# Performance work log

Hardware: AMD Instinct MI355X
Metric: run time of the kernel (lower is better)

The kernel has to match this reference:

```python
import jax, jax.numpy as jnp
import numpy as np
from jax.scipy.special import logsumexp

DEN_SCALE = 1.0  # den_scale from LFMMILoss.__init__


def _log_marginal(em, seqlens, logA, log_start, log_final):
    """Forward (alpha) recursion of a WFSA in log space.
    em: [B,T,S] per-state emission log-likelihoods; logA: [S,S] or [B,S,S].
    Returns per-sequence log-marginal [B].
    """
    B, T, S = em.shape
    alpha0 = log_start + em[:, 0]  # [B,S]

    def step(alpha, xs):
        em_t, t = xs
        # [B,S,1] + [.,S,S] -> logsumexp over source state
        new = logsumexp(alpha[:, :, None] + logA, axis=1) + em_t
        alpha = jnp.where((t < seqlens)[:, None], new, alpha)
        return alpha, None

    em_t_first = jnp.swapaxes(em, 0, 1)  # [T,B,S]
    alpha, _ = jax.lax.scan(step, alpha0, (em_t_first[1:], jnp.arange(1, T)))
    return logsumexp(alpha + log_final, axis=1)  # [B]


def _fsm_logprob(x, seqlens, logA, log_start, log_final, pdf_ids):
    B, T, _ = x.shape
    if pdf_ids.ndim == 1:  # shared graph (denominator)
        em = x[:, :, pdf_ids]  # [B,T,S]
    else:  # per-utterance graphs (numerators), pdf_ids: [B,S]
        S = pdf_ids.shape[-1]
        idx = jnp.broadcast_to(pdf_ids[:, None, :], (B, T, S))
        em = jnp.take_along_axis(x, idx, axis=2)
    return _log_marginal(em, seqlens, logA, log_start, log_final)


def setup_inputs() -> dict:
    key = jax.random.key(0)
    ks = jax.random.split(key, 10)
    B, T, C = 16, 500, 2048
    S_num, S_den = 64, 512
    inp = jax.random.normal(ks[0], (B, T, C), jnp.float32)
    seqlengths = jax.random.randint(ks[1], (B,), T // 2, T + 1, jnp.int32)
    num_logA = jax.nn.log_softmax(jax.random.normal(ks[2], (B, S_num, S_num), jnp.float32), axis=-1)
    num_log_start = jax.nn.log_softmax(jax.random.normal(ks[3], (B, S_num), jnp.float32), axis=-1)
    num_log_final = jax.nn.log_softmax(jax.random.normal(ks[4], (B, S_num), jnp.float32), axis=-1)
    num_pdf_ids = jax.random.randint(ks[5], (B, S_num), 0, C, jnp.int32)
    den_logA = jax.nn.log_softmax(jax.random.normal(ks[6], (S_den, S_den), jnp.float32), axis=-1)
    den_log_start = jax.nn.log_softmax(jax.random.normal(ks[7], (S_den,), jnp.float32), axis=-1)
    den_log_final = jax.nn.log_softmax(jax.random.normal(ks[8], (S_den,), jnp.float32), axis=-1)
    den_pdf_ids = jax.random.randint(ks[9], (S_den,), 0, C, jnp.int32)
    return {
        "input": inp, "seqlengths": seqlengths,
        "num_logA": num_logA, "num_log_start": num_log_start,
        "num_log_final": num_log_final, "num_pdf_ids": num_pdf_ids,
        "den_logA": den_logA, "den_log_start": den_log_start,
        "den_log_final": den_log_final, "den_pdf_ids": den_pdf_ids,
    }


def reference(input, seqlengths, num_logA, num_log_start, num_log_final,
              num_pdf_ids, den_logA, den_log_start, den_log_final, den_pdf_ids):
    x = jnp.clip(input, -30.0, 30.0)
    num_llh = _fsm_logprob(x, seqlengths, num_logA, num_log_start, num_log_final, num_pdf_ids).sum()
    den_llh = _fsm_logprob(x, seqlengths, den_logA, den_log_start, den_log_final, den_pdf_ids).sum()
    return -(num_llh - DEN_SCALE * den_llh)
```

## Files before the change

kernel.cpp:

```cpp
#include <hip/hip_runtime.h>
#include <math.h>

#define BB 16
#define TT 500
#define CC 2048
#define SN 64
#define SD 512
#define NDEN 128
#define NTHR 512
#define SHIFTC 30.0f

#define WSF_DACC   32768
#define WSF_DSCALE 32784
#define WSF_NACC   32800
#define WSF_NSCALE 32816

#define AL(p) __hip_atomic_load((p), __ATOMIC_RELAXED, __HIP_MEMORY_SCOPE_AGENT)
#define AS(p, v) __hip_atomic_store((p), (v), __ATOMIC_RELAXED, __HIP_MEMORY_SCOPE_AGENT)

__device__ __forceinline__ float wave_max(float v) {
  #pragma unroll
  for (int off = 32; off > 0; off >>= 1) v = fmaxf(v, __shfl_xor(v, off, 64));
  return v;
}
__device__ __forceinline__ float wave_sum(float v) {
  #pragma unroll
  for (int off = 32; off > 0; off >>= 1) v += __shfl_xor(v, off, 64);
  return v;
}
__device__ __forceinline__ unsigned long long pk(unsigned tag, float v) {
  return ((unsigned long long)tag << 32) | (unsigned long long)__float_as_uint(v);
}
__device__ __forceinline__ float clamp30(float v) {
  return fminf(fmaxf(v, -30.f), 30.f);
}

__global__ __launch_bounds__(NTHR, 1) void fsm_fwd(
    const float* __restrict__ x, const int* __restrict__ seqlens,
    const float* __restrict__ nA, const float* __restrict__ nls,
    const float* __restrict__ nlf, const int* __restrict__ npdf,
    const float* __restrict__ dA, const float* __restrict__ dls,
    const float* __restrict__ dlf, const int* __restrict__ dpdf,
    unsigned long long* __restrict__ p64, float* __restrict__ wsf)
{
  __shared__ float prt[2][8][64];
  __shared__ float pmx[2][8];
  const int tid = threadIdx.x;
  const int lane = tid & 63, wv = tid >> 6;

  if (blockIdx.x < NDEN) {
    const int g  = blockIdx.x & 15;
    const int cb = blockIdx.x >> 4;
    const int j0 = cb * 64;

    float Areg[64];
    {
      const float* Ap = dA + (size_t)(wv * 64) * SD + j0 + lane;
      #pragma unroll
      for (int k = 0; k < 64; ++k)
        Areg[k] = __expf(Ap[(size_t)k * SD]);
    }

    unsigned long long* gb0 = p64 + (size_t)g * SD;
    unsigned long long* gb1 = p64 + (size_t)(16 + g) * SD;

    const int si = j0 + lane;
    int pdfj = 0, sl = 0; float lfj = 0.f, pcur = 0.f, scale = SHIFTC;
    const float* xb = x + (size_t)g * TT * CC;
    if (wv == 0) {
      pdfj = dpdf[si];
      lfj  = dlf[si];
      sl   = seqlens[g];
      float xv = clamp30(xb[pdfj]);
      pcur = __expf(dls[si] + xv - SHIFTC);
      AS(gb0 + si, pk(0u, pcur));
    }
    float lmlag = 0.f;

    for (int t = 1; t < TT; ++t) {
      unsigned long long* gin  = (t & 1) ? gb0 : gb1;
      unsigned long long* gout = (t & 1) ? gb1 : gb0;

      float emfac = 0.f;
      if (wv == 0) {
        float xq = clamp30(xb[(size_t)t * CC + pdfj]);
        emfac = __expf(xq - SHIFTC - lmlag);
      }

      const unsigned tg = (unsigned)(t - 1);
      unsigned long long* pa = gin + wv * 64 + lane;
      float pwin;
      {
        unsigned long long w = AL(pa);
        for (;;) {
          unsigned long long wn = AL(pa);
          if ((unsigned)(w >> 32) == tg) {
            pwin = __uint_as_float((unsigned)w);
            break;
          }
          __builtin_amdgcn_s_sleep(1);
          w = wn;
        }
      }

      float q = 0.f;
      #pragma unroll
      for (int k = 0; k < 64; ++k) {
        float pv = __uint_as_float(__builtin_amdgcn_readlane(__float_as_uint(pwin), k));
        q = fmaf(pv, Areg[k], q);
      }
      prt[t & 1][wv][lane] = q;
      float cm = wave_max(pwin);
      if (lane == 0) pmx[t & 1][wv] = cm;
      __syncthreads();

      if (wv == 0) {
        float s = 0.f;
        #pragma unroll
        for (int r = 0; r < 8; ++r) s += prt[t & 1][r][lane];
        if (t < sl) {
          pcur = s * emfac;
          scale += SHIFTC + lmlag;
        }
        AS(gout + si, pk((unsigned)t, pcur));
        float m = pmx[t & 1][0];
        #pragma unroll
        for (int r = 1; r < 8; ++r) m = fmaxf(m, pmx[t & 1][r]);
        lmlag = __logf(m);
      }
    }
    if (wv == 0) {
      float part = wave_sum(pcur * __expf(lfj));
      if (lane == 0) {
        atomicAdd(wsf + WSF_DACC + g, part);
        if (cb == 0) wsf[WSF_DSCALE + g] = scale;
      }
    }
  } else {
    const int b = blockIdx.x - NDEN;
    if (wv != 0) return;

    float Areg[64];
    {
      const float* Ap = nA + b * SN * SN + lane;
      #pragma unroll
      for (int i = 0; i < 64; ++i)
        Areg[i] = __expf(Ap[i * SN]);
    }
    const int   pdfj = npdf[b * SN + lane];
    const float lfj  = nlf[b * SN + lane];
    const int   sl   = seqlens[b];
    float xv = clamp30(x[(size_t)b * TT * CC + pdfj]);
    float pcur = __expf(nls[b * SN + lane] + xv - SHIFTC);
    float scale = SHIFTC;

    for (int t = 1; t < TT; ++t) {
      xv = clamp30(x[(size_t)b * TT * CC + t * CC + pdfj]);
      float pold = pcur;
      float q = 0.f;
      #pragma unroll
      for (int i = 0; i < 64; ++i) {
        float pi = __uint_as_float(__builtin_amdgcn_readlane(__float_as_uint(pold), i));
        q = fmaf(pi, Areg[i], q);
      }
      float lm = __logf(wave_max(pold));
      if (t < sl) {
        pcur = q * __expf(xv - SHIFTC - lm);
        scale += SHIFTC + lm;
      }
    }
    float part = wave_sum(pcur * __expf(lfj));
    if (lane == 0) {
      wsf[WSF_NACC + b]   = part;
      wsf[WSF_NSCALE + b] = scale;
    }
  }
}

__global__ void fsm_final(const float* __restrict__ wsf, float* __restrict__ out) {
  const int tid = threadIdx.x;
  float v = 0.f;
  if (tid < 16)
    v = -(wsf[WSF_NSCALE + tid] + __logf(wsf[WSF_NACC + tid]));
  else if (tid < 32)
    v = (wsf[WSF_DSCALE + tid - 16] + __logf(wsf[WSF_DACC + tid - 16]));
  v = wave_sum(v);
  if (tid == 0) out[0] = v;
}

extern "C" void kernel_launch(void* const* d_in, const int* in_sizes, int n_in,
                              void* d_out, int out_size, void* d_ws, size_t ws_size,
                              hipStream_t stream) {
  const float* x    = (const float*)d_in[0];
  const int*   sql  = (const int*)d_in[1];
  const float* nA   = (const float*)d_in[2];
  const float* nls  = (const float*)d_in[3];
  const float* nlf  = (const float*)d_in[4];
  const int*   npdf = (const int*)d_in[5];
  const float* dA   = (const float*)d_in[6];
  const float* dls  = (const float*)d_in[7];
  const float* dlf  = (const float*)d_in[8];
  const int*   dpdf = (const int*)d_in[9];
  float* out = (float*)d_out;
  unsigned long long* p64 = (unsigned long long*)d_ws;
  float* wsf = (float*)d_ws;
  (void)in_sizes; (void)n_in; (void)out_size; (void)ws_size;

  hipMemsetAsync((char*)d_ws + 131072, 0, 256, stream);
  fsm_fwd<<<NDEN + BB, NTHR, 0, stream>>>(x, sql, nA, nls, nlf, npdf,
                                          dA, dls, dlf, dpdf, p64, wsf);
  fsm_final<<<1, 64, 0, stream>>>(wsf, out);
}
```

Baseline: 932.9 us.

## Add fast SE-scope exchange path with device-scope fallback for cross-block alpha handoff

Each denominator timestep's alpha values are now written twice: to a buffer using sc0 (shader-engine/L2-near) stores and to a device-scope buffer using sc1. Consumers poll the fast buffer first and fall back to the device-scope copy every few spins. Fast buffers are initialised with a sentinel tag. The goal is lower latency in the per-step inter-block handoff, which sets the pace of the serial recursion. The cost is an extra store per step and reliance on cache-coherence semantics that depend on which blocks share a shader engine.

After: 1.132 ms. 21.3% more time.

```diff
diff --git a/kernel.cpp b/kernel.cpp
--- a/kernel.cpp
+++ b/kernel.cpp
@@ -9,14 +9,32 @@
 #define NDEN 128
 #define NTHR 512
 #define SHIFTC 30.0f
-
-#define WSF_DACC   32768
-#define WSF_DSCALE 32784
-#define WSF_NACC   32800
-#define WSF_NSCALE 32816
-
-#define AL(p) __hip_atomic_load((p), __ATOMIC_RELAXED, __HIP_MEMORY_SCOPE_AGENT)
-#define AS(p, v) __hip_atomic_store((p), (v), __ATOMIC_RELAXED, __HIP_MEMORY_SCOPE_AGENT)
+#define SENT 0xFFFFFFFF00000000ull
+
+#define SLOWO 16384
+#define WSF_DACC   65536
+#define WSF_DSCALE 65552
+#define WSF_NACC   65568
+#define WSF_NSCALE 65584
+
+__device__ __forceinline__ void st_se(unsigned long long* p, unsigned long long v) {
+  asm volatile("global_store_dwordx2 %0, %1, off sc0" :: "v"(p), "v"(v) : "memory");
+}
+__device__ __forceinline__ unsigned long long ld_se(const unsigned long long* p) {
+  unsigned long long r;
+  asm volatile("global_load_dwordx2 %0, %1, off sc0\n\ts_waitcnt vmcnt(0)"
+               : "=v"(r) : "v"(p) : "memory");
+  return r;
+}
+__device__ __forceinline__ void st_dev(unsigned long long* p, unsigned long long v) {
+  asm volatile("global_store_dwordx2 %0, %1, off sc1" :: "v"(p), "v"(v) : "memory");
+}
+__device__ __forceinline__ unsigned long long ld_dev(const unsigned long long* p) {
+  unsigned long long r;
+  asm volatile("global_load_dwordx2 %0, %1, off sc1\n\ts_waitcnt vmcnt(0)"
+               : "=v"(r) : "v"(p) : "memory");
+  return r;
+}
 
 __device__ __forceinline__ float wave_max(float v) {
   #pragma unroll
@@ -53,6 +71,14 @@
     const int cb = blockIdx.x >> 4;
     const int j0 = cb * 64;
 
+    unsigned long long* fb0 = p64 + (size_t)g * SD;
+    unsigned long long* fb1 = p64 + (size_t)(16 + g) * SD;
+    unsigned long long* sb0 = p64 + SLOWO + (size_t)g * SD;
+    unsigned long long* sb1 = p64 + SLOWO + (size_t)(16 + g) * SD;
+
+    st_se(fb0 + wv * 64 + lane, SENT);
+    st_se(fb1 + wv * 64 + lane, SENT);
+
     float Areg[64];
     {
       const float* Ap = dA + (size_t)(wv * 64) * SD + j0 + lane;
@@ -60,9 +86,7 @@
       for (int k = 0; k < 64; ++k)
         Areg[k] = __expf(Ap[(size_t)k * SD]);
     }
-
-    unsigned long long* gb0 = p64 + (size_t)g * SD;
-    unsigned long long* gb1 = p64 + (size_t)(16 + g) * SD;
+    __syncthreads();
 
     const int si = j0 + lane;
     int pdfj = 0, sl = 0; float lfj = 0.f, pcur = 0.f, scale = SHIFTC;
@@ -73,13 +97,16 @@
       sl   = seqlens[g];
       float xv = clamp30(xb[pdfj]);
       pcur = __expf(dls[si] + xv - SHIFTC);
-      AS(gb0 + si, pk(0u, pcur));
+      st_dev(sb0 + si, pk(0u, pcur));
     }
     float lmlag = 0.f;
 
     for (int t = 1; t < TT; ++t) {
-      unsigned long long* gin  = (t & 1) ? gb0 : gb1;
-      unsigned long long* gout = (t & 1) ? gb1 : gb0;
+      const int bi = t & 1;
+      unsigned long long* fin  = bi ? fb0 : fb1;
+      unsigned long long* sin  = bi ? sb0 : sb1;
+      unsigned long long* fout = bi ? fb1 : fb0;
+      unsigned long long* sout = bi ? sb1 : sb0;
 
       float emfac = 0.f;
       if (wv == 0) {
@@ -88,44 +115,54 @@
       }
 
       const unsigned tg = (unsigned)(t - 1);
-      unsigned long long* pa = gin + wv * 64 + lane;
-      float pwin;
-      {
-        unsigned long long w = AL(pa);
+      unsigned long long* fa = fin + wv * 64 + lane;
+      unsigned long long* sa = sin + wv * 64 + lane;
+      unsigned long long w;
+      if (t == 1) {
         for (;;) {
-          unsigned long long wn = AL(pa);
-          if ((unsigned)(w >> 32) == tg) {
-            pwin = __uint_as_float((unsigned)w);
-            break;
+          w = ld_dev(sa);
+          if ((unsigned)(w >> 32) == tg) break;
+          __builtin_amdgcn_s_sleep(1);
+        }
+      } else {
+        int k = 0;
+        for (;;) {
+          w = ld_se(fa);
+          if ((unsigned)(w >> 32) == tg) break;
+          if ((++k & 3) == 0) {
+            w = ld_dev(sa);
+            if ((unsigned)(w >> 32) == tg) break;
+            __builtin_amdgcn_s_sleep(1);
           }
-          __builtin_amdgcn_s_sleep(1);
-          w = wn;
         }
       }
+      float pwin = __uint_as_float((unsigned)w);
 
       float q = 0.f;
       #pragma unroll
-      for (int k = 0; k < 64; ++k) {
-        float pv = __uint_as_float(__builtin_amdgcn_readlane(__float_as_uint(pwin), k));
-        q = fmaf(pv, Areg[k], q);
-      }
-      prt[t & 1][wv][lane] = q;
+      for (int k2 = 0; k2 < 64; ++k2) {
+        float pv = __uint_as_float(__builtin_amdgcn_readlane(__float_as_uint(pwin), k2));
+        q = fmaf(pv, Areg[k2], q);
+      }
+      prt[bi][wv][lane] = q;
       float cm = wave_max(pwin);
-      if (lane == 0) pmx[t & 1][wv] = cm;
+      if (lane == 0) pmx[bi][wv] = cm;
       __syncthreads();
 
       if (wv == 0) {
         float s = 0.f;
         #pragma unroll
-        for (int r = 0; r < 8; ++r) s += prt[t & 1][r][lane];
+        for (int r = 0; r < 8; ++r) s += prt[bi][r][lane];
         if (t < sl) {
           pcur = s * emfac;
           scale += SHIFTC + lmlag;
         }
-        AS(gout + si, pk((unsigned)t, pcur));
-        float m = pmx[t & 1][0];
+        unsigned long long w64 = pk((unsigned)t, pcur);
+        st_se(fout + si, w64);
+        st_dev(sout + si, w64);
+        float m = pmx[bi][0];
         #pragma unroll
-        for (int r = 1; r < 8; ++r) m = fmaxf(m, pmx[t & 1][r]);
+        for (int r = 1; r < 8; ++r) m = fmaxf(m, pmx[bi][r]);
         lmlag = __logf(m);
       }
     }
@@ -155,7 +192,7 @@
     float scale = SHIFTC;
 
     for (int t = 1; t < TT; ++t) {
-      xv = clamp30(x[(size_t)b * TT * CC + t * CC + pdfj]);
+      xv = clamp30(x[(size_t)b * TT * CC + (size_t)t * CC + pdfj]);
       float pold = pcur;
       float q = 0.f;
       #pragma unroll
@@ -206,7 +243,7 @@
   float* wsf = (float*)d_ws;
   (void)in_sizes; (void)n_in; (void)out_size; (void)ws_size;
 
-  hipMemsetAsync((char*)d_ws + 131072, 0, 256, stream);
+  hipMemsetAsync((char*)d_ws + 262144, 0, 256, stream);
   fsm_fwd<<<NDEN + BB, NTHR, 0, stream>>>(x, sql, nA, nls, nlf, npdf,
                                           dA, dls, dlf, dpdf, p64, wsf);
   fsm_final<<<1, 64, 0, stream>>>(wsf, out);
```
